# Performance work log

Measured on AMD Instinct MI355X. Metric: run time of the kernel, lower is better.

Reference implementation:

```python
import jax, jax.numpy as jnp
import numpy as np

KW = 3          # kernel_width
PAD = (KW - 1) // 2


def setup_inputs() -> dict:
    key = jax.random.key(0)
    ks = jax.random.split(key, 7)
    B, QL, KL, QS, KS = 16, 1024, 1024, 512, 512
    q = jax.random.normal(ks[0], (B, QL, QS), dtype=jnp.float32)
    k = jax.random.normal(ks[1], (B, KL, KS), dtype=jnp.float32)
    # torch Linear weights: [out_features, in_features]
    Wk = jax.random.normal(ks[2], (KS * KW, QS), dtype=jnp.float32) * (1.0 / np.sqrt(QS))
    bk = jax.random.normal(ks[3], (KS * KW,), dtype=jnp.float32) * 0.02
    Wb = jax.random.normal(ks[4], (1, QS), dtype=jnp.float32) * (1.0 / np.sqrt(QS))
    bb = jax.random.normal(ks[5], (1,), dtype=jnp.float32) * 0.02
    bias_b = jax.random.normal(ks[6], (1,), dtype=jnp.float32)
    return {"q": q, "k": k, "Wk": Wk, "bk": bk, "Wb": Wb, "bb": bb, "bias_b": bias_b}


def reference(q, k, Wk, bk, Wb, bb, bias_b):
    B, QL, QS = q.shape
    _, KL, KS = k.shape
    # per-query dynamic kernels: [B, QL, KS, KW]
    kernel = (jnp.einsum('biq,oq->bio', q, Wk) + bk).reshape(B, QL, KS, KW)
    # per-query scalar bias: [B, QL]
    bias = (jnp.einsum('biq,oq->bio', q, Wb) + bb)[..., 0]
    # banded multiply-accumulate, equivalent to grouped conv1d with groups=B
    k_pad = jnp.pad(k, ((0, 0), (PAD, PAD), (0, 0)))  # [B, KL+KW-1, KS]
    # windows[b, j, t, c] = k_pad[b, j+t, c]  -> [B, KL, KW, KS]
    windows = jnp.stack([k_pad[:, t:t + KL, :] for t in range(KW)], axis=2)
    scores = jnp.einsum('bict,bjtc->bij', kernel, windows)
    return scores + bias[:, :, None] + bias_b[0]
```

## Files before the change

### kernel.cpp

```cpp
#include <hip/hip_runtime.h>

typedef unsigned short ushort_t;
typedef unsigned int uint32;
typedef __bf16 bf16x8 __attribute__((ext_vector_type(8)));
typedef float f32x4 __attribute__((ext_vector_type(4)));
typedef float f4 __attribute__((ext_vector_type(4)));
typedef unsigned short us4 __attribute__((ext_vector_type(4)));


__device__ __forceinline__ ushort_t f2bf(float f) {
    uint32 u = __builtin_bit_cast(uint32, f);
    u = (u + 0x7fffu + ((u >> 16) & 1u)) >> 16;
    return (ushort_t)u;
}

#define FULL_BAR() do { __builtin_amdgcn_sched_barrier(0); __builtin_amdgcn_s_barrier(); __builtin_amdgcn_sched_barrier(0); } while (0)
#define HALF_BAR() do { __builtin_amdgcn_sched_barrier(0); __builtin_amdgcn_s_barrier(); } while (0)
#define PRE_MFMA() do { __builtin_amdgcn_sched_barrier(0); __builtin_amdgcn_s_barrier(); \
    asm volatile("s_waitcnt lgkmcnt(0)" ::: "memory"); __builtin_amdgcn_sched_barrier(0); } while (0)

#define AS1 __attribute__((address_space(1)))
#define AS3 __attribute__((address_space(3)))

__global__ __launch_bounds__(256) void prep_all(const float* __restrict__ q,
                                                const float* __restrict__ Wb,
                                                const float* __restrict__ bb,
                                                const float* __restrict__ k,
                                                const float* __restrict__ Wk,
                                                const float* __restrict__ bk,
                                                ushort_t* __restrict__ qb,
                                                float* __restrict__ biasw,
                                                ushort_t* __restrict__ kbp,
                                                ushort_t* __restrict__ wkb,
                                                float* __restrict__ bkp) {
    const int tid = threadIdx.x;
    if (blockIdx.x < 4096) {
        const int lane = tid & 63, wid = tid >> 6;
        const int m = blockIdx.x * 4 + wid;
        const float* qrow = q + (size_t)m * 512;

        f4 v0 = *(const f4*)(qrow + lane * 4);
        f4 v1 = *(const f4*)(qrow + 256 + lane * 4);
        f4 w0 = *(const f4*)(Wb + lane * 4);
        f4 w1 = *(const f4*)(Wb + 256 + lane * 4);

        float dot = v0[0]*w0[0] + v0[1]*w0[1] + v0[2]*w0[2] + v0[3]*w0[3]
                  + v1[0]*w1[0] + v1[1]*w1[1] + v1[2]*w1[2] + v1[3]*w1[3];

        us4 o0, o1;
        o0[0]=f2bf(v0[0]); o0[1]=f2bf(v0[1]); o0[2]=f2bf(v0[2]); o0[3]=f2bf(v0[3]);
        o1[0]=f2bf(v1[0]); o1[1]=f2bf(v1[1]); o1[2]=f2bf(v1[2]); o1[3]=f2bf(v1[3]);
        *(us4*)(qb + (size_t)m * 512 + lane * 4) = o0;
        *(us4*)(qb + (size_t)m * 512 + 256 + lane * 4) = o1;

        #pragma unroll
        for (int off = 32; off >= 1; off >>= 1) dot += __shfl_xor(dot, off);
        if (lane == 0) biasw[m] = dot + bb[0];
        return;
    }
    const int gid = (blockIdx.x - 4096) * 256 + tid;
    if (gid < 1536) bkp[gid] = bk[(gid & 511) * 3 + (gid >> 9)];

    const int KG = (16 * 1024 * 512) / 4;
    const int PG = (16 * 2 * 512) / 4;

    if (gid < KG) {
        const int e = gid * 4;
        const int b = e >> 19;
        const int rem = e & ((1 << 19) - 1);
        const int row = rem >> 9, c = rem & 511;
        f4 v = *(const f4*)(k + e);
        us4 o; o[0]=f2bf(v[0]); o[1]=f2bf(v[1]); o[2]=f2bf(v[2]); o[3]=f2bf(v[3]);
        *(us4*)(kbp + ((size_t)b * 1026 + row + 1) * 512 + c) = o;
    } else if (gid < KG + PG) {
        const int p = gid - KG;
        const int b = p >> 8, off = p & 255;
        const int row = (off < 128) ? 0 : 1025;
        const int c = (off & 127) * 4;
        us4 z; z[0]=0; z[1]=0; z[2]=0; z[3]=0;
        *(us4*)(kbp + ((size_t)b * 1026 + row) * 512 + c) = z;
    } else {
        const int w = gid - KG - PG;
        const int n = w >> 7;
        const int c = (w & 127) * 4;
        const int o = (n & 511) * 3 + (n >> 9);
        f4 v = *(const f4*)(Wk + (size_t)o * 512 + c);
        us4 ov; ov[0]=f2bf(v[0]); ov[1]=f2bf(v[1]); ov[2]=f2bf(v[2]); ov[3]=f2bf(v[3]);
        *(us4*)(wkb + (size_t)n * 512 + c) = ov;
    }
}

template<int NINST>
__device__ __forceinline__ void stage_half(const char* base, int ld, char* dst, int tid) {
    #pragma unroll
    for (int inst = 0; inst < NINST; ++inst) {
        const int idx = inst * 512 + tid;
        const int row = idx >> 2;
        const int scol = ((idx & 3) ^ ((row >> 1) & 3)) << 4;
        __builtin_amdgcn_global_load_lds(
            (const AS1 void*)(base + (size_t)row * (size_t)ld + scol),
            (AS3 void*)(dst + (size_t)(inst * 512 + (tid & ~63)) * 16),
            16, 0, 0);
    }
}

#define MFMA_CLUSTER(af, bf, accrow)                                         \
    __builtin_amdgcn_s_setprio(1);                                           \
    _Pragma("unroll")                                                        \
    for (int i_ = 0; i_ < 4; ++i_)                                           \
        _Pragma("unroll")                                                    \
        for (int j_ = 0; j_ < 4; ++j_)                                       \
            acc[(accrow) + i_][j_] = __builtin_amdgcn_mfma_f32_16x16x32_bf16( \
                af[i_], bf[j_], acc[(accrow) + i_][j_], 0, 0, 0);            \
    __builtin_amdgcn_s_setprio(0);

__global__ __launch_bounds__(512) void gemm1(const ushort_t* __restrict__ qb,
                                             const ushort_t* __restrict__ wkb,
                                             const float* __restrict__ bkp,
                                             ushort_t* __restrict__ coef) {
    __shared__ alignas(16) char lds[98304];
    const int tid = threadIdx.x;
    const int l = tid & 63, wid = tid >> 6;
    const int wr = wid >> 2, wc = wid & 3;
    int bid = blockIdx.x;
    bid = (bid & 7) * 96 + (bid >> 3);
    const int mt = bid & 127, nt = bid >> 7;
    const int mbase = mt * 128, nbase = nt * 256;

    const char* Ag = (const char*)(qb + (size_t)mbase * 512);
    const char* Bg = (const char*)(wkb + (size_t)nbase * 512);

    const int r15 = l & 15, q = l >> 4;
    const int swz = ((q ^ (r15 >> 1)) & 3) << 4;
    const int laneA = (wr * 64 + r15) * 64 + swz;
    const int laneB = (wc * 64 + r15) * 64 + swz;

    f32x4 acc[4][4];
    #pragma unroll
    for (int mi = 0; mi < 4; ++mi)
        #pragma unroll
        for (int ni = 0; ni < 4; ++ni)
            #pragma unroll
            for (int r = 0; r < 4; ++r) acc[mi][ni][r] = 0.f;

    stage_half<1>(Ag, 1024, lds, tid);
    stage_half<2>(Bg, 1024, lds + 16384, tid);
    stage_half<1>(Ag + 64, 1024, lds + 8192, tid);
    stage_half<2>(Bg + 64, 1024, lds + 32768, tid);
    asm volatile("s_waitcnt vmcnt(3)" ::: "memory");
    FULL_BAR();

    for (int t = 0; t < 8; ++t) {
        const char* bA = lds + ((t & 1) ? 49152 : 0);
        char* nb = lds + ((t & 1) ? 0 : 49152);
        const int tn = (t < 7) ? t + 1 : t;
        const size_t off = (size_t)tn * 128;

        bf16x8 a0[4], b0[4];
        #pragma unroll
        for (int i = 0; i < 4; ++i) a0[i] = *(const bf16x8*)(bA + laneA + i * 1024);
        #pragma unroll
        for (int j = 0; j < 4; ++j) b0[j] = *(const bf16x8*)(bA + 16384 + laneB + j * 1024);
        stage_half<1>(Ag + off, 1024, nb, tid);
        stage_half<2>(Bg + off, 1024, nb + 16384, tid);
        asm volatile("s_waitcnt vmcnt(3)" ::: "memory");
        PRE_MFMA();
        MFMA_CLUSTER(a0, b0, 0)
        HALF_BAR();

        bf16x8 a1[4], b1[4];
        #pragma unroll
        for (int i = 0; i < 4; ++i) a1[i] = *(const bf16x8*)(bA + 8192 + laneA + i * 1024);
        #pragma unroll
        for (int j = 0; j < 4; ++j) b1[j] = *(const bf16x8*)(bA + 32768 + laneB + j * 1024);
        stage_half<1>(Ag + off + 64, 1024, nb + 8192, tid);
        stage_half<2>(Bg + off + 64, 1024, nb + 32768, tid);
        asm volatile("s_waitcnt vmcnt(3)" ::: "memory");
        PRE_MFMA();
        MFMA_CLUSTER(a1, b1, 0)
        HALF_BAR();
    }

    #pragma unroll
    for (int ni = 0; ni < 4; ++ni) {
        const int ncol = nbase + wc * 64 + ni * 16 + r15;
        const float bkv = bkp[ncol];
        #pragma unroll
        for (int mi = 0; mi < 4; ++mi) {
            const int mrow0 = mbase + wr * 64 + mi * 16 + q * 4;
            #pragma unroll
            for (int r = 0; r < 4; ++r)
                coef[(size_t)(mrow0 + r) * 1536 + ncol] = f2bf(acc[mi][ni][r] + bkv);
        }
    }
}

__global__ __launch_bounds__(512) void gemm2(const ushort_t* __restrict__ coef,
                                             const ushort_t* __restrict__ kbp,
                                             const float* __restrict__ biasw,
                                             const float* __restrict__ bias_b,
                                             float* __restrict__ out) {
    __shared__ alignas(16) char lds[131072];
    const int tid = threadIdx.x;
    const int l = tid & 63, wid = tid >> 6;
    const int wr = wid >> 2, wc = wid & 3;
    int bid = blockIdx.x;
    bid = (bid & 7) * 32 + (bid >> 3);
    const int jt = bid & 3, it = (bid >> 2) & 3, b = bid >> 4;
    const int ibase = it * 256, jbase = jt * 256;

    const char* Ag = (const char*)(coef + ((size_t)b * 1024 + ibase) * 1536);
    const char* Bg = (const char*)(kbp + ((size_t)b * 1026 + jbase) * 512);

    const int r15 = l & 15, q = l >> 4;
    const int swz = ((q ^ (r15 >> 1)) & 3) << 4;
    const int laneA = (wr * 128 + r15) * 64 + swz;
    const int laneB = (wc * 64 + r15) * 64 + swz;

    f32x4 acc[8][4];
    #pragma unroll
    for (int mi = 0; mi < 8; ++mi)
        #pragma unroll
        for (int ni = 0; ni < 4; ++ni)
            #pragma unroll
            for (int r = 0; r < 4; ++r) acc[mi][ni][r] = 0.f;

    stage_half<2>(Ag, 3072, lds, tid);
    stage_half<2>(Bg, 1024, lds + 32768, tid);
    stage_half<2>(Ag + 64, 3072, lds + 16384, tid);
    stage_half<2>(Bg + 64, 1024, lds + 49152, tid);
    asm volatile("s_waitcnt vmcnt(4)" ::: "memory");
    FULL_BAR();

    for (int t = 0; t < 24; ++t) {
        const char* bA = lds + ((t & 1) << 16);
        char* nb = lds + (((t + 1) & 1) << 16);
        const int tn = (t < 23) ? t + 1 : t;
        const size_t aoff = (size_t)tn * 128;
        const size_t boff = (size_t)(tn >> 3) * 1024 + (size_t)(tn & 7) * 128;

        bf16x8 a0[4], b0[4];
        #pragma unroll
        for (int i = 0; i < 4; ++i) a0[i] = *(const bf16x8*)(bA + laneA + i * 1024);
        #pragma unroll
        for (int j = 0; j < 4; ++j) b0[j] = *(const bf16x8*)(bA + 32768 + laneB + j * 1024);
        stage_half<2>(Ag + aoff, 3072, nb, tid);
        PRE_MFMA();
        MFMA_CLUSTER(a0, b0, 0)
        HALF_BAR();

        bf16x8 a1[4];
        #pragma unroll
        for (int i = 0; i < 4; ++i) a1[i] = *(const bf16x8*)(bA + laneA + (4 + i) * 1024);
        stage_half<2>(Bg + boff, 1024, nb + 32768, tid);
        asm volatile("s_waitcnt vmcnt(4)" ::: "memory");
        PRE_MFMA();
        MFMA_CLUSTER(a1, b0, 4)
        HALF_BAR();

        bf16x8 a2[4], b1[4];
        #pragma unroll
        for (int i = 0; i < 4; ++i) a2[i] = *(const bf16x8*)(bA + 16384 + laneA + i * 1024);
        #pragma unroll
        for (int j = 0; j < 4; ++j) b1[j] = *(const bf16x8*)(bA + 49152 + laneB + j * 1024);
        stage_half<2>(Ag + aoff + 64, 3072, nb + 16384, tid);
        PRE_MFMA();
        MFMA_CLUSTER(a2, b1, 0)
        HALF_BAR();

        bf16x8 a3[4];
        #pragma unroll
        for (int i = 0; i < 4; ++i) a3[i] = *(const bf16x8*)(bA + 16384 + laneA + (4 + i) * 1024);
        stage_half<2>(Bg + boff + 64, 1024, nb + 49152, tid);
        asm volatile("s_waitcnt vmcnt(4)" ::: "memory");
        PRE_MFMA();
        MFMA_CLUSTER(a3, b1, 4)
        HALF_BAR();
    }

    const float bb0v = bias_b[0];
    #pragma unroll
    for (int mi = 0; mi < 8; ++mi) {
        const int irow0 = ibase + wr * 128 + mi * 16 + q * 4;
        #pragma unroll
        for (int r = 0; r < 4; ++r) {
            const float bv = biasw[b * 1024 + irow0 + r] + bb0v;
            #pragma unroll
            for (int ni = 0; ni < 4; ++ni) {
                const int jcol = jbase + wc * 64 + ni * 16 + r15;
                out[((size_t)b << 20) + (size_t)(irow0 + r) * 1024 + jcol] = acc[mi][ni][r] + bv;
            }
        }
    }
}

extern "C" void kernel_launch(void* const* d_in, const int* in_sizes, int n_in,
                              void* d_out, int out_size, void* d_ws, size_t ws_size,
                              hipStream_t stream) {
    const float* q      = (const float*)d_in[0];
    const float* k      = (const float*)d_in[1];
    const float* Wk     = (const float*)d_in[2];
    const float* bk     = (const float*)d_in[3];
    const float* Wb     = (const float*)d_in[4];
    const float* bb     = (const float*)d_in[5];
    const float* bias_b = (const float*)d_in[6];
    float* out = (float*)d_out;

    ushort_t* ws   = (ushort_t*)d_ws;
    ushort_t* qb   = ws;
    ushort_t* kbp  = qb  + (size_t)16384 * 512;
    ushort_t* wkb  = kbp + (size_t)16 * 1026 * 512;
    ushort_t* coef = wkb + (size_t)1536 * 512;
    float*    biasw = (float*)(coef + (size_t)16384 * 1536);
    float*    bkp   = biasw + 16384;

    prep_all<<<13072, 256, 0, stream>>>(q, Wb, bb, k, Wk, bk, qb, biasw, kbp, wkb, bkp);
    gemm1<<<768, 512, 0, stream>>>(qb, wkb, bkp, coef);
    gemm2<<<256, 512, 0, stream>>>(coef, kbp, biasw, bias_b, out);
}
```

Before: 216.7 us.

## Software-pipeline LDS fragment loads across MFMA blocks in both GEMMs

Restructures both GEMM main loops so the LDS fragment loads for the next MFMA block are issued before the current block runs, using register double-buffering (Aa/Ab, Ba/Bb) and fewer barriers per iteration. gemm1 moves from a double-buffered to a triple-buffered LDS ring (147 KB) with a two-tile prefetch distance. Both kernels add a launch_bounds occupancy hint. The aim is to hide LDS and global latency behind MFMA work; the risks are higher register pressure and harder-to-verify barrier and vmcnt correctness.

```diff
diff --git a/kernel.cpp b/kernel.cpp
--- a/kernel.cpp
+++ b/kernel.cpp
@@ -14,10 +14,8 @@
     return (ushort_t)u;
 }
 
-#define FULL_BAR() do { __builtin_amdgcn_sched_barrier(0); __builtin_amdgcn_s_barrier(); __builtin_amdgcn_sched_barrier(0); } while (0)
-#define HALF_BAR() do { __builtin_amdgcn_sched_barrier(0); __builtin_amdgcn_s_barrier(); } while (0)
-#define PRE_MFMA() do { __builtin_amdgcn_sched_barrier(0); __builtin_amdgcn_s_barrier(); \
-    asm volatile("s_waitcnt lgkmcnt(0)" ::: "memory"); __builtin_amdgcn_sched_barrier(0); } while (0)
+#define SB0() __builtin_amdgcn_sched_barrier(0)
+#define SBAR() __builtin_amdgcn_s_barrier()
 
 #define AS1 __attribute__((address_space(1)))
 #define AS3 __attribute__((address_space(3)))
@@ -104,21 +102,25 @@
     }
 }
 
-#define MFMA_CLUSTER(af, bf, accrow)                                         \
+#define MFMA_BLK(af, bf, r0, NM)                                             \
+    SB0();                                                                   \
     __builtin_amdgcn_s_setprio(1);                                           \
     _Pragma("unroll")                                                        \
-    for (int i_ = 0; i_ < 4; ++i_)                                           \
+    for (int i_ = 0; i_ < (NM); ++i_)                                        \
         _Pragma("unroll")                                                    \
         for (int j_ = 0; j_ < 4; ++j_)                                       \
-            acc[(accrow) + i_][j_] = __builtin_amdgcn_mfma_f32_16x16x32_bf16( \
-                af[i_], bf[j_], acc[(accrow) + i_][j_], 0, 0, 0);            \
-    __builtin_amdgcn_s_setprio(0);
-
-__global__ __launch_bounds__(512) void gemm1(const ushort_t* __restrict__ qb,
-                                             const ushort_t* __restrict__ wkb,
-                                             const float* __restrict__ bkp,
-                                             ushort_t* __restrict__ coef) {
-    __shared__ alignas(16) char lds[98304];
+            acc[(r0) + i_][j_] = __builtin_amdgcn_mfma_f32_16x16x32_bf16(    \
+                af[i_], bf[j_], acc[(r0) + i_][j_], 0, 0, 0);                \
+    __builtin_amdgcn_s_setprio(0);                                           \
+    SB0();
+
+#define VMCNT(n) asm volatile("s_waitcnt vmcnt(" #n ")" ::: "memory")
+
+__global__ __launch_bounds__(512, 2) void gemm1(const ushort_t* __restrict__ qb,
+                                                const ushort_t* __restrict__ wkb,
+                                                const float* __restrict__ bkp,
+                                                ushort_t* __restrict__ coef) {
+    __shared__ alignas(16) char lds[147456];
     const int tid = threadIdx.x;
     const int l = tid & 63, wid = tid >> 6;
     const int wr = wid >> 2, wc = wid & 3;
@@ -147,38 +149,53 @@
     stage_half<2>(Bg, 1024, lds + 16384, tid);
     stage_half<1>(Ag + 64, 1024, lds + 8192, tid);
     stage_half<2>(Bg + 64, 1024, lds + 32768, tid);
-    asm volatile("s_waitcnt vmcnt(3)" ::: "memory");
-    FULL_BAR();
+    stage_half<1>(Ag + 128, 1024, lds + 49152, tid);
+    stage_half<2>(Bg + 128, 1024, lds + 49152 + 16384, tid);
+    stage_half<1>(Ag + 192, 1024, lds + 49152 + 8192, tid);
+    stage_half<2>(Bg + 192, 1024, lds + 49152 + 32768, tid);
+    VMCNT(9);
+    SBAR();
+    bf16x8 Aa[2], Ab[2], Ba[4], Bb[4];
+    #pragma unroll
+    for (int i = 0; i < 2; ++i) Aa[i] = *(const bf16x8*)(lds + laneA + i * 1024);
+    #pragma unroll
+    for (int j = 0; j < 4; ++j) Ba[j] = *(const bf16x8*)(lds + 16384 + laneB + j * 1024);
 
     for (int t = 0; t < 8; ++t) {
-        const char* bA = lds + ((t & 1) ? 49152 : 0);
-        char* nb = lds + ((t & 1) ? 0 : 49152);
-        const int tn = (t < 7) ? t + 1 : t;
-        const size_t off = (size_t)tn * 128;
-
-        bf16x8 a0[4], b0[4];
-        #pragma unroll
-        for (int i = 0; i < 4; ++i) a0[i] = *(const bf16x8*)(bA + laneA + i * 1024);
-        #pragma unroll
-        for (int j = 0; j < 4; ++j) b0[j] = *(const bf16x8*)(bA + 16384 + laneB + j * 1024);
-        stage_half<1>(Ag + off, 1024, nb, tid);
-        stage_half<2>(Bg + off, 1024, nb + 16384, tid);
-        asm volatile("s_waitcnt vmcnt(3)" ::: "memory");
-        PRE_MFMA();
-        MFMA_CLUSTER(a0, b0, 0)
-        HALF_BAR();
-
-        bf16x8 a1[4], b1[4];
-        #pragma unroll
-        for (int i = 0; i < 4; ++i) a1[i] = *(const bf16x8*)(bA + 8192 + laneA + i * 1024);
-        #pragma unroll
-        for (int j = 0; j < 4; ++j) b1[j] = *(const bf16x8*)(bA + 32768 + laneB + j * 1024);
-        stage_half<1>(Ag + off + 64, 1024, nb + 8192, tid);
-        stage_half<2>(Bg + off + 64, 1024, nb + 32768, tid);
-        asm volatile("s_waitcnt vmcnt(3)" ::: "memory");
-        PRE_MFMA();
-        MFMA_CLUSTER(a1, b1, 0)
-        HALF_BAR();
+        const char* R  = lds + (t % 3) * 49152;
+        const char* Nx = lds + ((t + 1) % 3) * 49152;
+        char* W        = lds + ((t + 2) % 3) * 49152;
+        const int tn2 = (t + 2 < 8) ? t + 2 : 7;
+        const size_t off2 = (size_t)tn2 * 128;
+
+        #pragma unroll
+        for (int i = 0; i < 2; ++i) Ab[i] = *(const bf16x8*)(R + laneA + (2 + i) * 1024);
+        SB0(); SBAR();
+        MFMA_BLK(Aa, Ba, 0, 2)
+
+        stage_half<1>(Ag + off2, 1024, W, tid);
+        stage_half<2>(Bg + off2, 1024, W + 16384, tid);
+        VMCNT(6);
+        SBAR(); SB0();
+        #pragma unroll
+        for (int i = 0; i < 2; ++i) Aa[i] = *(const bf16x8*)(R + 8192 + laneA + i * 1024);
+        #pragma unroll
+        for (int j = 0; j < 4; ++j) Bb[j] = *(const bf16x8*)(R + 32768 + laneB + j * 1024);
+        MFMA_BLK(Ab, Ba, 2, 2)
+
+        stage_half<1>(Ag + off2 + 64, 1024, W + 8192, tid);
+        stage_half<2>(Bg + off2 + 64, 1024, W + 32768, tid);
+        #pragma unroll
+        for (int i = 0; i < 2; ++i) Ab[i] = *(const bf16x8*)(R + 8192 + laneA + (2 + i) * 1024);
+        MFMA_BLK(Aa, Bb, 0, 2)
+
+        VMCNT(6);
+        SBAR(); SB0();
+        #pragma unroll
+        for (int i = 0; i < 2; ++i) Aa[i] = *(const bf16x8*)(Nx + laneA + i * 1024);
+        #pragma unroll
+        for (int j = 0; j < 4; ++j) Ba[j] = *(const bf16x8*)(Nx + 16384 + laneB + j * 1024);
+        MFMA_BLK(Ab, Bb, 2, 2)
     }
 
     #pragma unroll
@@ -195,11 +212,11 @@
     }
 }
 
-__global__ __launch_bounds__(512) void gemm2(const ushort_t* __restrict__ coef,
-                                             const ushort_t* __restrict__ kbp,
-                                             const float* __restrict__ biasw,
-                                             const float* __restrict__ bias_b,
-                                             float* __restrict__ out) {
+__global__ __launch_bounds__(512, 2) void gemm2(const ushort_t* __restrict__ coef,
+                                                const ushort_t* __restrict__ kbp,
+                                                const float* __restrict__ biasw,
+                                                const float* __restrict__ bias_b,
+                                                float* __restrict__ out) {
     __shared__ alignas(16) char lds[131072];
     const int tid = threadIdx.x;
     const int l = tid & 63, wid = tid >> 6;
@@ -229,53 +246,49 @@
     stage_half<2>(Bg, 1024, lds + 32768, tid);
     stage_half<2>(Ag + 64, 3072, lds + 16384, tid);
     stage_half<2>(Bg + 64, 1024, lds + 49152, tid);
-    asm volatile("s_waitcnt vmcnt(4)" ::: "memory");
-    FULL_BAR();
+    VMCNT(4);
+    SBAR();
+    bf16x8 Aa[4], Ab[4], Ba[4], Bb[4];
+    #pragma unroll
+    for (int i = 0; i < 4; ++i) Aa[i] = *(const bf16x8*)(lds + laneA + i * 1024);
+    #pragma unroll
+    for (int j = 0; j < 4; ++j) Ba[j] = *(const bf16x8*)(lds + 32768 + laneB + j * 1024);
 
     for (int t = 0; t < 24; ++t) {
-        const char* bA = lds + ((t & 1) << 16);
-        char* nb = lds + (((t + 1) & 1) << 16);
+        const char* R = lds + ((t & 1) << 16);
+        char* W       = lds + (((t + 1) & 1) << 16);
         const int tn = (t < 23) ? t + 1 : t;
         const size_t aoff = (size_t)tn * 128;
         const size_t boff = (size_t)(tn >> 3) * 1024 + (size_t)(tn & 7) * 128;
 
-        bf16x8 a0[4], b0[4];
-        #pragma unroll
-        for (int i = 0; i < 4; ++i) a0[i] = *(const bf16x8*)(bA + laneA + i * 1024);
-        #pragma unroll
-        for (int j = 0; j < 4; ++j) b0[j] = *(const bf16x8*)(bA + 32768 + laneB + j * 1024);
-        stage_half<2>(Ag + aoff, 3072, nb, tid);
-        PRE_MFMA();
-        MFMA_CLUSTER(a0, b0, 0)
-        HALF_BAR();
-
-        bf16x8 a1[4];
-        #pragma unroll
-        for (int i = 0; i < 4; ++i) a1[i] = *(const bf16x8*)(bA + laneA + (4 + i) * 1024);
-        stage_half<2>(Bg + boff, 1024, nb + 32768, tid);
-        asm volatile("s_waitcnt vmcnt(4)" ::: "memory");
-        PRE_MFMA();
-        MFMA_CLUSTER(a1, b0, 4)
-        HALF_BAR();
-
-        bf16x8 a2[4], b1[4];
-        #pragma unroll
-        for (int i = 0; i < 4; ++i) a2[i] = *(const bf16x8*)(bA + 16384 + laneA + i * 1024);
-        #pragma unroll
-        for (int j = 0; j < 4; ++j) b1[j] = *(const bf16x8*)(bA + 49152 + laneB + j * 1024);
-        stage_half<2>(Ag + aoff + 64, 3072, nb + 16384, tid);
-        PRE_MFMA();
-        MFMA_CLUSTER(a2, b1, 0)
-        HALF_BAR();
-
-        bf16x8 a3[4];
-        #pragma unroll
-        for (int i = 0; i < 4; ++i) a3[i] = *(const bf16x8*)(bA + 16384 + laneA + (4 + i) * 1024);
-        stage_half<2>(Bg + boff + 64, 1024, nb + 49152, tid);
-        asm volatile("s_waitcnt vmcnt(4)" ::: "memory");
-        PRE_MFMA();
-        MFMA_CLUSTER(a3, b1, 4)
-        HALF_BAR();
+        #pragma unroll
+        for (int i = 0; i < 4; ++i) Ab[i] = *(const bf16x8*)(R + laneA + (4 + i) * 1024);
+        SB0(); SBAR();
+        MFMA_BLK(Aa, Ba, 0, 4)
+
+        stage_half<2>(Ag + aoff, 3072, W, tid);
+        stage_half<2>(Bg + boff, 1024, W + 32768, tid);
+        VMCNT(4);
+        SBAR(); SB0();
+        #pragma unroll
+        for (int i = 0; i < 4; ++i) Aa[i] = *(const bf16x8*)(R + 16384 + laneA + i * 1024);
+        #pragma unroll
+        for (int j = 0; j < 4; ++j) Bb[j] = *(const bf16x8*)(R + 49152 + laneB + j * 1024);
+        MFMA_BLK(Ab, Ba, 4, 4)
+
+        stage_half<2>(Ag + aoff + 64, 3072, W + 16384, tid);
+        stage_half<2>(Bg + boff + 64, 1024, W + 49152, tid);
+        #pragma unroll
+        for (int i = 0; i < 4; ++i) Ab[i] = *(const bf16x8*)(R + 16384 + laneA + (4 + i) * 1024);
+        MFMA_BLK(Aa, Bb, 0, 4)
+
+        VMCNT(4);
+        SBAR(); SB0();
+        #pragma unroll
+        for (int i = 0; i < 4; ++i) Aa[i] = *(const bf16x8*)(W + laneA + i * 1024);
+        #pragma unroll
+        for (int j = 0; j < 4; ++j) Ba[j] = *(const bf16x8*)(W + 32768 + laneB + j * 1024);
+        MFMA_BLK(Ab, Bb, 4, 4)
     }
 
     const float bb0v = bias_b[0];
```

Measured after the change: 217.4 us. Within noise of the previous version (+0.3%).
